# Performance work log

Hardware: AMD Instinct MI355X
Metric: run time of the kernel (lower is better)

## Reference

```python
import jax, jax.numpy as jnp
import numpy as np


def setup_inputs() -> dict:
    key = jax.random.key(0)
    kx, ks = jax.random.split(key)
    X = jax.random.normal(kx, (8, 4096, 16), dtype=jnp.float32)
    # nn.Parameter(torch.rand(1) + 1.0)
    sigma = jax.random.uniform(ks, (1,), dtype=jnp.float32) + 1.0
    return {"X": X, "sigma": sigma}


def reference(X, sigma):
    sq = jnp.sum(X * X, axis=-1)                       # [B, N]
    inner = jnp.einsum('bnf,bmf->bnm', X, X)           # [B, N, N]
    sqdist = sq[:, :, None] + sq[:, None, :] - 2.0 * inner
    sqdist = jnp.maximum(sqdist, 0.0)                  # guard tiny negatives
    gaussian = jnp.exp(-sqdist / sigma[0])             # [B, N, N]
    # original _softmax: exp(gaussian) / sum over dim 2 == softmax over axis 2
    return jax.nn.softmax(gaussian, axis=2)
```

## Files before the change

kernel.cpp:

```cpp
#include <hip/hip_runtime.h>


constexpr int Bn  = 8;
constexpr int N   = 4096;
constexpr int F   = 16;
constexpr int TN  = 4;
constexpr int BLK = 512;
constexpr int WPB = BLK / 64;

__device__ __forceinline__ float dot4(float4 a, float4 b) {
    return fmaf(a.x, b.x, fmaf(a.y, b.y, fmaf(a.z, b.z, a.w * b.w)));
}

__global__ __launch_bounds__(BLK, 4)
void gaussian_softmax_kernel(const float* __restrict__ X,
                             const float* __restrict__ sigma_p,
                             float* __restrict__ out) {
    __shared__ float lds_e[TN][N];
    __shared__ float red[TN][WPB];

    const int tid = threadIdx.x;
    const int b   = blockIdx.y;
    const int n0  = blockIdx.x * TN;
    const float* Xb = X + (size_t)b * N * F;

    float4 q0[TN], q1[TN], q2[TN], q3[TN];
    float  sqn[TN];
    #pragma unroll
    for (int r = 0; r < TN; ++r) {
        const float4* qp = (const float4*)(Xb + (size_t)(n0 + r) * F);
        q0[r] = qp[0]; q1[r] = qp[1]; q2[r] = qp[2]; q3[r] = qp[3];
        sqn[r] = dot4(q0[r], q0[r]) + dot4(q1[r], q1[r])
               + dot4(q2[r], q2[r]) + dot4(q3[r], q3[r]);
    }

    const float neg_inv_sigma = -1.0f / sigma_p[0];

    float sum[TN];
    #pragma unroll
    for (int r = 0; r < TN; ++r) sum[r] = 0.f;

    #pragma unroll 2
    for (int it = 0; it < N / BLK; ++it) {
        const int m = it * BLK + tid;
        const float4* xmp = (const float4*)(Xb + (size_t)m * F);
        const float4 a0 = xmp[0], a1 = xmp[1], a2 = xmp[2], a3 = xmp[3];

        const float sqm = dot4(a0, a0) + dot4(a1, a1) + dot4(a2, a2) + dot4(a3, a3);

        #pragma unroll
        for (int r = 0; r < TN; ++r) {
            float d = dot4(q0[r], a0) + dot4(q1[r], a1)
                    + dot4(q2[r], a2) + dot4(q3[r], a3);
            float sqd = fmaf(-2.0f, d, sqn[r] + sqm);
            sqd = fmaxf(sqd, 0.0f);
            float g = __expf(sqd * neg_inv_sigma);
            float e = __expf(g);
            lds_e[r][m] = e;
            sum[r] += e;
        }
    }

    #pragma unroll
    for (int r = 0; r < TN; ++r) {
        float s = sum[r];
        #pragma unroll
        for (int off = 32; off > 0; off >>= 1) s += __shfl_down(s, off, 64);
        if ((tid & 63) == 0) red[r][tid >> 6] = s;
    }
    __syncthreads();

    float inv[TN];
    #pragma unroll
    for (int r = 0; r < TN; ++r) {
        float t = 0.f;
        #pragma unroll
        for (int w = 0; w < WPB; ++w) t += red[r][w];
        inv[r] = 1.0f / t;
    }

    float* outb = out + ((size_t)b * N + (size_t)n0) * (size_t)N;
    #pragma unroll
    for (int r = 0; r < TN; ++r) {
        #pragma unroll
        for (int j = 0; j < N / (BLK * 4); ++j) {
            const int c = j * (BLK * 4) + tid * 4;
            float4 v = *(const float4*)&lds_e[r][c];
            v.x *= inv[r]; v.y *= inv[r]; v.z *= inv[r]; v.w *= inv[r];
            *(float4*)&outb[(size_t)r * N + c] = v;
        }
    }
}

extern "C" void kernel_launch(void* const* d_in, const int* in_sizes, int n_in,
                              void* d_out, int out_size, void* d_ws, size_t ws_size,
                              hipStream_t stream) {
    const float* X     = (const float*)d_in[0];
    const float* sigma = (const float*)d_in[1];
    float* out         = (float*)d_out;

    dim3 grid(N / TN, Bn);
    dim3 block(BLK);
    gaussian_softmax_kernel<<<grid, block, 0, stream>>>(X, sigma, out);
}
```

Measured before the change: 617.9 us.

## Transpose X into feature-major workspace and hold exponentials in registers

A pre-pass kernel writes X in feature-major order so each thread of the main kernel can read four consecutive columns per feature with float4 loads. The main kernel keeps its computed exponentials in registers instead of a 64 KB LDS buffer, which frees LDS and allows more blocks per CU. Query values and sigma are made wave-uniform with readfirstlane so they can stay in scalar registers. The cost is one extra kernel launch, a workspace round trip, and higher VGPR pressure from the per-thread register array.

New measurement: 1.441 ms. 133% more time.

```diff
diff --git a/kernel.cpp b/kernel.cpp
--- a/kernel.cpp
+++ b/kernel.cpp
@@ -1,22 +1,39 @@
 #include <hip/hip_runtime.h>
 
 
-constexpr int Bn  = 8;
-constexpr int N   = 4096;
-constexpr int F   = 16;
-constexpr int TN  = 4;
-constexpr int BLK = 512;
-constexpr int WPB = BLK / 64;
+constexpr int Bn   = 8;
+constexpr int N    = 4096;
+constexpr int F    = 16;
+constexpr int TN   = 4;
+constexpr int BLK  = 512;
+constexpr int ITERS = N / (BLK * 4);
+constexpr int WPB  = BLK / 64;
 
-__device__ __forceinline__ float dot4(float4 a, float4 b) {
-    return fmaf(a.x, b.x, fmaf(a.y, b.y, fmaf(a.z, b.z, a.w * b.w)));
+__global__ __launch_bounds__(256)
+void pack_kernel(const float* __restrict__ X, float* __restrict__ Xt) {
+    const int b = blockIdx.y;
+    const int m = blockIdx.x * 256 + threadIdx.x;
+    const float4* src = (const float4*)(X + ((size_t)b * N + m) * F);
+    const float4 v0 = src[0], v1 = src[1], v2 = src[2], v3 = src[3];
+    const float x[F] = {v0.x, v0.y, v0.z, v0.w, v1.x, v1.y, v1.z, v1.w,
+                        v2.x, v2.y, v2.z, v2.w, v3.x, v3.y, v3.z, v3.w};
+    float* dst = Xt + (size_t)b * F * N + m;
+    #pragma unroll
+    for (int f = 0; f < F; ++f) dst[(size_t)f * N] = x[f];
+}
+
+__device__ __forceinline__ float uni(float x) {
+    return __int_as_float(__builtin_amdgcn_readfirstlane(__float_as_int(x)));
+}
+
+__device__ __forceinline__ float gse(float d, float base, float nis) {
+    float sqd = fmaxf(fmaf(-2.0f, d, base), 0.0f);
+    return __expf(__expf(sqd * nis));
 }
 
 __global__ __launch_bounds__(BLK, 4)
-void gaussian_softmax_kernel(const float* __restrict__ X,
-                             const float* __restrict__ sigma_p,
-                             float* __restrict__ out) {
-    __shared__ float lds_e[TN][N];
+void gs_main(const float* __restrict__ X, const float* __restrict__ Xt,
+             const float* __restrict__ sigma_p, float* __restrict__ out) {
     __shared__ float red[TN][WPB];
 
     const int tid = threadIdx.x;
@@ -24,40 +41,60 @@
     const int n0  = blockIdx.x * TN;
     const float* Xb = X + (size_t)b * N * F;
 
-    float4 q0[TN], q1[TN], q2[TN], q3[TN];
-    float  sqn[TN];
+    float q[TN][F];
+    float sqn[TN];
     #pragma unroll
     for (int r = 0; r < TN; ++r) {
-        const float4* qp = (const float4*)(Xb + (size_t)(n0 + r) * F);
-        q0[r] = qp[0]; q1[r] = qp[1]; q2[r] = qp[2]; q3[r] = qp[3];
-        sqn[r] = dot4(q0[r], q0[r]) + dot4(q1[r], q1[r])
-               + dot4(q2[r], q2[r]) + dot4(q3[r], q3[r]);
+        float s = 0.f;
+        #pragma unroll
+        for (int f = 0; f < F; ++f) {
+            float qq = uni(Xb[(size_t)(n0 + r) * F + f]);
+            q[r][f] = qq;
+            s = fmaf(qq, qq, s);
+        }
+        sqn[r] = s;
     }
+    const float nis = -1.0f / uni(sigma_p[0]);
 
-    const float neg_inv_sigma = -1.0f / sigma_p[0];
+    const float4* Xt4 = (const float4*)(Xt + (size_t)b * F * N);
 
-    float sum[TN];
+    float4 e4[TN][ITERS];
+    float  sum[TN] = {0.f, 0.f, 0.f, 0.f};
+
     #pragma unroll
-    for (int r = 0; r < TN; ++r) sum[r] = 0.f;
+    for (int it = 0; it < ITERS; ++it) {
+        const int c4 = it * BLK + tid;
 
-    #pragma unroll 2
-    for (int it = 0; it < N / BLK; ++it) {
-        const int m = it * BLK + tid;
-        const float4* xmp = (const float4*)(Xb + (size_t)m * F);
-        const float4 a0 = xmp[0], a1 = xmp[1], a2 = xmp[2], a3 = xmp[3];
+        float4 d[TN];
+        #pragma unroll
+        for (int r = 0; r < TN; ++r) d[r] = make_float4(0.f, 0.f, 0.f, 0.f);
+        float4 sq = make_float4(0.f, 0.f, 0.f, 0.f);
 
-        const float sqm = dot4(a0, a0) + dot4(a1, a1) + dot4(a2, a2) + dot4(a3, a3);
+        #pragma unroll
+        for (int f = 0; f < F; ++f) {
+            const float4 v = Xt4[(size_t)f * (N / 4) + c4];
+            sq.x = fmaf(v.x, v.x, sq.x);
+            sq.y = fmaf(v.y, v.y, sq.y);
+            sq.z = fmaf(v.z, v.z, sq.z);
+            sq.w = fmaf(v.w, v.w, sq.w);
+            #pragma unroll
+            for (int r = 0; r < TN; ++r) {
+                d[r].x = fmaf(q[r][f], v.x, d[r].x);
+                d[r].y = fmaf(q[r][f], v.y, d[r].y);
+                d[r].z = fmaf(q[r][f], v.z, d[r].z);
+                d[r].w = fmaf(q[r][f], v.w, d[r].w);
+            }
+        }
 
         #pragma unroll
         for (int r = 0; r < TN; ++r) {
-            float d = dot4(q0[r], a0) + dot4(q1[r], a1)
-                    + dot4(q2[r], a2) + dot4(q3[r], a3);
-            float sqd = fmaf(-2.0f, d, sqn[r] + sqm);
-            sqd = fmaxf(sqd, 0.0f);
-            float g = __expf(sqd * neg_inv_sigma);
-            float e = __expf(g);
-            lds_e[r][m] = e;
-            sum[r] += e;
+            float4 e;
+            e.x = gse(d[r].x, sqn[r] + sq.x, nis);
+            e.y = gse(d[r].y, sqn[r] + sq.y, nis);
+            e.z = gse(d[r].z, sqn[r] + sq.z, nis);
+            e.w = gse(d[r].w, sqn[r] + sq.w, nis);
+            e4[r][it] = e;
+            sum[r] += (e.x + e.y) + (e.z + e.w);
         }
     }
 
@@ -79,15 +116,14 @@
         inv[r] = 1.0f / t;
     }
 
-    float* outb = out + ((size_t)b * N + (size_t)n0) * (size_t)N;
+    float* outb = out + ((size_t)b * N + n0) * (size_t)N;
     #pragma unroll
     for (int r = 0; r < TN; ++r) {
         #pragma unroll
-        for (int j = 0; j < N / (BLK * 4); ++j) {
-            const int c = j * (BLK * 4) + tid * 4;
-            float4 v = *(const float4*)&lds_e[r][c];
+        for (int it = 0; it < ITERS; ++it) {
+            float4 v = e4[r][it];
             v.x *= inv[r]; v.y *= inv[r]; v.z *= inv[r]; v.w *= inv[r];
-            *(float4*)&outb[(size_t)r * N + c] = v;
+            ((float4*)(outb + (size_t)r * N))[it * BLK + tid] = v;
         }
     }
 }
@@ -98,8 +134,8 @@
     const float* X     = (const float*)d_in[0];
     const float* sigma = (const float*)d_in[1];
     float* out         = (float*)d_out;
+    float* Xt          = (float*)d_ws;
 
-    dim3 grid(N / TN, Bn);
-    dim3 block(BLK);
-    gaussian_softmax_kernel<<<grid, block, 0, stream>>>(X, sigma, out);
+    pack_kernel<<<dim3(N / 256, Bn), 256, 0, stream>>>(X, Xt);
+    gs_main<<<dim3(N / TN, Bn), BLK, 0, stream>>>(X, Xt, sigma, out);
 }
```
